# Performance work log

Measured on AMD Instinct MI355X. Metric: run time of the kernel, lower is better.

The kernel has to match this reference:

```python
import jax, jax.numpy as jnp
import numpy as np
from jax import lax

R = 1
EPS = 1e-4
K = 2 * R + 1


def _dir_kernels(r):
    k = 2 * r + 1
    ones = np.ones((k, k), np.float32)
    L = ones.copy(); L[:, r + 1:] = 0
    Rk = ones.copy(); Rk[:, :r] = 0
    U = ones.copy(); U[r + 1:, :] = 0
    D = ones.copy(); D[:r, :] = 0
    # NW/NE/SW/SE clone U/D BEFORE normalization (as in the torch code)
    NW = U.copy(); NW[:, r + 1:] = 0
    NE = U.copy(); NE[:, :r] = 0
    SW = D.copy(); SW[:, r + 1:] = 0
    SE = D.copy(); SE[:, :r] = 0
    half = (r + 1) * k          # normalizer for half windows
    quad = (r + 1) ** 2         # normalizer for quadrant windows
    L, Rk, U, D = L / half, Rk / half, U / half, D / half
    NW, NE, SW, SE = NW / quad, NE / quad, SW / quad, SE / quad
    return jnp.asarray(np.stack([L, Rk, U, D, NW, NE, SW, SE])[:, None])  # [8,1,k,k]


_DN = ('NCHW', 'OIHW', 'NCHW')


def _boxfilter(x, r):
    # replication pad + depthwise ones/(k*k) box filter; x: [N,3,H,W]
    k = 2 * r + 1
    xp = jnp.pad(x, ((0, 0), (0, 0), (r, r), (r, r)), mode='edge')
    w = jnp.full((3, 1, k, k), 1.0 / (k * k), dtype=x.dtype)
    return lax.conv_general_dilated(xp, w, (1, 1), 'VALID',
                                    dimension_numbers=_DN, feature_group_count=3)


def setup_inputs() -> dict:
    key = jax.random.key(0)
    k1, k2, k3 = jax.random.split(key, 3)
    lr_x = jax.random.uniform(k1, (1, 3, 2048, 2048), jnp.float32) * 255.0
    lr_y = jax.random.uniform(k2, (1, 3, 2048, 2048), jnp.float32) * 255.0
    hr_x = jax.random.uniform(k3, (1, 3, 4096, 4096), jnp.float32) * 255.0
    return {"lr_x": lr_x, "lr_y": lr_y, "hr_x": hr_x}


def reference(lr_x, lr_y, hr_x):
    # guided-filter coefficients on the low-res pair
    mean_x = _boxfilter(lr_x, R)
    mean_y = _boxfilter(lr_y, R)
    cov_xy = _boxfilter(lr_x * lr_y, R) - mean_x * mean_y
    var_x = _boxfilter(lr_x * lr_x, R) - mean_x * mean_x
    A = cov_xy / (var_x + EPS)            # [1,3,H,W]
    b = mean_y - A * mean_x               # [1,3,H,W]

    # treat channels as batch: [3,1,H,W]; 8 directional kernels at once
    Wd = _dir_kernels(R)                  # [8,1,k,k]
    A_ = A[0][:, None]
    b_ = b[0][:, None]
    im = lr_x[0][:, None]                 # [3,1,H,W]
    pad = [(R, R), (R, R)]
    convA = lax.conv_general_dilated(A_, Wd, (1, 1), pad, dimension_numbers=_DN)
    convb = lax.conv_general_dilated(b_, Wd, (1, 1), pad, dimension_numbers=_DN)
    d = convA * im + convb - im           # [3,8,H,W] directional residuals

    idx = jnp.argmin(jnp.abs(d), axis=1, keepdims=True)   # [3,1,H,W]
    dm = jnp.take_along_axis(d, idx, axis=1)              # best residual
    res = (dm + im).transpose(1, 0, 2, 3)                 # [1,3,H,W]
    # .int() truncation then clamp to [0,255], back to float
    return jnp.clip(jnp.trunc(res), 0.0, 255.0)
```

## Files before the change

### kernel.cpp

```cpp
#include <hip/hip_runtime.h>
#include <math.h>


#define TX 64
#define TY 16
#define SW (TX + 4)
#define SH (TY + 4)
#define AW (TX + 2)
#define AH (TY + 2)
#define NT 256

#define NA (AH * AW)
#define NV (AH * SW)
#define NS (SH * SW)
#define ITER_A ((NA + NT - 1) / NT)

__device__ __forceinline__ double fast_rcp(double v) {
#if __has_builtin(__builtin_amdgcn_rcp)
    double r = __builtin_amdgcn_rcp(v);
#else
    double r = 1.0 / v;
#endif
    double e = fma(-v, r, 1.0);
    r = fma(r, e, r);
    e = fma(-v, r, 1.0);
    r = fma(r, e, r);
    return r;
}

__global__ __launch_bounds__(NT) void fgf_fused_kernel(
    const float* __restrict__ x, const float* __restrict__ y,
    float* __restrict__ out, int H, int W)
{
    __shared__ float  sxs[SH][SW];
    __shared__ float  sys[SH][SW];
    __shared__ double sV[4][AH][SW];

    const int c   = blockIdx.z;
    const int ox0 = blockIdx.x * TX;
    const int oy0 = blockIdx.y * TY;
    const size_t plane = (size_t)H * (size_t)W;
    const float* xc = x + (size_t)c * plane;
    const float* yc = y + (size_t)c * plane;

    const int tid = threadIdx.y * 64 + threadIdx.x;

    for (int i = tid; i < NS; i += NT) {
        int ly = i / SW, lx = i - ly * SW;
        int gy = oy0 - 2 + ly;
        int gx = ox0 - 2 + lx;
        gy = gy < 0 ? 0 : (gy >= H ? H - 1 : gy);
        gx = gx < 0 ? 0 : (gx >= W ? W - 1 : gx);
        size_t gidx = (size_t)gy * W + gx;
        sxs[ly][lx] = xc[gidx];
        sys[ly][lx] = yc[gidx];
    }
    __syncthreads();

    for (int i = tid; i < NV; i += NT) {
        int ly = i / SW, lx = i - ly * SW;
        double x0 = (double)sxs[ly + 0][lx];
        double x1 = (double)sxs[ly + 1][lx];
        double x2 = (double)sxs[ly + 2][lx];
        double y0 = (double)sys[ly + 0][lx];
        double y1 = (double)sys[ly + 1][lx];
        double y2 = (double)sys[ly + 2][lx];
        sV[0][ly][lx] = (x0 + x1) + x2;
        sV[1][ly][lx] = (y0 + y1) + y2;
        sV[2][ly][lx] = fma(x2, y2, fma(x1, y1, x0 * y0));
        sV[3][ly][lx] = fma(x2, x2, fma(x1, x1, x0 * x0));
    }
    __syncthreads();

    const double EPS81 = 81.0 * 1.0e-4;
    const double INV9  = 1.0 / 9.0;
    double Abuf[ITER_A], Bbuf[ITER_A];
#pragma unroll
    for (int it = 0; it < ITER_A; it++) {
        int i = tid + it * NT;
        double Av = 0.0, Bv = 0.0;
        if (i < NA) {
            int ly = i / AW, lx = i - ly * AW;
            int ay = oy0 - 1 + ly;
            int ax = ox0 - 1 + lx;
            if (ay >= 0 && ay < H && ax >= 0 && ax < W) {
                double Sx  = (sV[0][ly][lx] + sV[0][ly][lx + 1]) + sV[0][ly][lx + 2];
                double Sy  = (sV[1][ly][lx] + sV[1][ly][lx + 1]) + sV[1][ly][lx + 2];
                double Sxy = (sV[2][ly][lx] + sV[2][ly][lx + 1]) + sV[2][ly][lx + 2];
                double Sxx = (sV[3][ly][lx] + sV[3][ly][lx + 1]) + sV[3][ly][lx + 2];
                double num = fma(9.0, Sxy, -(Sx * Sy));
                double den = fma(-Sx, Sx, fma(9.0, Sxx, EPS81));
                Av = num * fast_rcp(den);
                Bv = fma(-Av, Sx, Sy) * INV9;
            }
        }
        Abuf[it] = Av;
        Bbuf[it] = Bv;
    }
    __syncthreads();
#pragma unroll
    for (int it = 0; it < ITER_A; it++) {
        int i = tid + it * NT;
        if (i < NA) {
            int ly = i / AW, lx = i - ly * AW;
            sV[0][ly][lx] = Abuf[it];
            sV[1][ly][lx] = Bbuf[it];
        }
    }
    __syncthreads();

    double (*sA)[SW] = sV[0];
    double (*sB)[SW] = sV[1];

    const double I6 = 1.0 / 6.0;
    const int tx = threadIdx.x;
    const int g  = threadIdx.y;
    const int r0 = g * 4;
    const int xg = ox0 + tx;
    const bool xok = (xg < W);

    double tLA, tRA, tFA, mLA, mRA, mFA, pLA, pRA, pFA;
    double tLB, tRB, tFB, mLB, mRB, mFB, pLB, pRB, pFB;
    {
        double a0 = sA[r0 + 0][tx], a1 = sA[r0 + 0][tx + 1], a2 = sA[r0 + 0][tx + 2];
        double L0 = a0 + a1, R0 = a1 + a2, F0 = L0 + a2;
        a0 = sA[r0 + 1][tx]; a1 = sA[r0 + 1][tx + 1]; a2 = sA[r0 + 1][tx + 2];
        double L1 = a0 + a1, R1 = a1 + a2, F1 = L1 + a2;
        a0 = sA[r0 + 2][tx]; a1 = sA[r0 + 2][tx + 1]; a2 = sA[r0 + 2][tx + 2];
        double L2 = a0 + a1, R2 = a1 + a2, F2 = L2 + a2;
        tLA = L0 + L1; tRA = R0 + R1; tFA = F0 + F1;
        mLA = L1 + L2; mRA = R1 + R2; mFA = F1 + F2;
        pLA = L2; pRA = R2; pFA = F2;

        double b0 = sB[r0 + 0][tx], b1 = sB[r0 + 0][tx + 1], b2 = sB[r0 + 0][tx + 2];
        double M0 = b0 + b1, S0 = b1 + b2, G0 = M0 + b2;
        b0 = sB[r0 + 1][tx]; b1 = sB[r0 + 1][tx + 1]; b2 = sB[r0 + 1][tx + 2];
        double M1 = b0 + b1, S1 = b1 + b2, G1 = M1 + b2;
        b0 = sB[r0 + 2][tx]; b1 = sB[r0 + 2][tx + 1]; b2 = sB[r0 + 2][tx + 2];
        double M2 = b0 + b1, S2 = b1 + b2, G2 = M2 + b2;
        tLB = M0 + M1; tRB = S0 + S1; tFB = G0 + G1;
        mLB = M1 + M2; mRB = S1 + S2; mFB = G1 + G2;
        pLB = M2; pRB = S2; pFB = G2;
    }

#pragma unroll
    for (int step = 0; step < 4; step++) {
        const int r  = r0 + step;
        const int yg = oy0 + r;
        if (xok && yg < H) {
            double im  = (double)sxs[r + 2][tx + 2];
            double mim = -im;

            double sa[8] = { tLA + pLA, tRA + pRA, tFA, mFA, tLA, tRA, mLA, mRA };
            double sb[8] = { tLB + pLB, tRB + pRB, tFB, mFB, tLB, tRB, mLB, mRB };

            double best = 0.0;
#pragma unroll
            for (int k = 0; k < 8; k++) {
                double w = (k < 4) ? I6 : 0.25;
                double d = fma(w, fma(sa[k], im, sb[k]), mim);
                if (k == 0) best = d;
                else        best = (fabs(d) < fabs(best)) ? d : best;
            }

            double res = trunc(best + im);
            res = fmin(fmax(res, 0.0), 255.0);
            out[(size_t)c * plane + (size_t)yg * W + xg] = (float)res;
        }

        if (step < 3) {
            double n0 = sA[r + 3][tx], n1 = sA[r + 3][tx + 1], n2 = sA[r + 3][tx + 2];
            double nL = n0 + n1, nR = n1 + n2, nF = nL + n2;
            tLA = mLA; tRA = mRA; tFA = mFA;
            mLA = pLA + nL; mRA = pRA + nR; mFA = pFA + nF;
            pLA = nL; pRA = nR; pFA = nF;

            n0 = sB[r + 3][tx]; n1 = sB[r + 3][tx + 1]; n2 = sB[r + 3][tx + 2];
            nL = n0 + n1; nR = n1 + n2; nF = nL + n2;
            tLB = mLB; tRB = mRB; tFB = mFB;
            mLB = pLB + nL; mRB = pRB + nR; mFB = pFB + nF;
            pLB = nL; pRB = nR; pFB = nF;
        }
    }
}

extern "C" void kernel_launch(void* const* d_in, const int* in_sizes, int n_in,
                              void* d_out, int out_size, void* d_ws, size_t ws_size,
                              hipStream_t stream) {
    const float* lr_x = (const float*)d_in[0];
    const float* lr_y = (const float*)d_in[1];
    float* out = (float*)d_out;

    const int plane = in_sizes[0] / 3;
    const int H = (int)(0.5 + sqrt((double)plane));
    const int W = plane / H;

    dim3 block(64, 4, 1);
    dim3 grid((W + TX - 1) / TX, (H + TY - 1) / TY, 3);
    fgf_fused_kernel<<<grid, block, 0, stream>>>(lr_x, lr_y, out, H, W);
}
```

Measured before the change: 386.9 us.

## Halve tile height, drop float staging tiles, read vertical sums from global

```diff
diff --git a/kernel.cpp b/kernel.cpp
--- a/kernel.cpp
+++ b/kernel.cpp
@@ -3,16 +3,16 @@
 
 
 #define TX 64
-#define TY 16
+#define TY 8
 #define SW (TX + 4)
-#define SH (TY + 4)
+#define AH (TY + 2)
 #define AW (TX + 2)
-#define AH (TY + 2)
 #define NT 256
-
+#define STEPS 2
+
+#define NV (AH * SW)
 #define NA (AH * AW)
-#define NV (AH * SW)
-#define NS (SH * SW)
+#define ITER_V ((NV + NT - 1) / NT)
 #define ITER_A ((NA + NT - 1) / NT)
 
 __device__ __forceinline__ double fast_rcp(double v) {
@@ -28,12 +28,14 @@
     return r;
 }
 
-__global__ __launch_bounds__(NT) void fgf_fused_kernel(
+__device__ __forceinline__ int iclamp(int v, int lo, int hi) {
+    return v < lo ? lo : (v > hi ? hi : v);
+}
+
+__global__ __launch_bounds__(NT, 7) void fgf_fused_kernel(
     const float* __restrict__ x, const float* __restrict__ y,
     float* __restrict__ out, int H, int W)
 {
-    __shared__ float  sxs[SH][SW];
-    __shared__ float  sys[SH][SW];
     __shared__ double sV[4][AH][SW];
 
     const int c   = blockIdx.z;
@@ -43,32 +45,40 @@
     const float* xc = x + (size_t)c * plane;
     const float* yc = y + (size_t)c * plane;
 
-    const int tid = threadIdx.y * 64 + threadIdx.x;
-
-    for (int i = tid; i < NS; i += NT) {
-        int ly = i / SW, lx = i - ly * SW;
-        int gy = oy0 - 2 + ly;
-        int gx = ox0 - 2 + lx;
-        gy = gy < 0 ? 0 : (gy >= H ? H - 1 : gy);
-        gx = gx < 0 ? 0 : (gx >= W ? W - 1 : gx);
-        size_t gidx = (size_t)gy * W + gx;
-        sxs[ly][lx] = xc[gidx];
-        sys[ly][lx] = yc[gidx];
-    }
-    __syncthreads();
-
-    for (int i = tid; i < NV; i += NT) {
-        int ly = i / SW, lx = i - ly * SW;
-        double x0 = (double)sxs[ly + 0][lx];
-        double x1 = (double)sxs[ly + 1][lx];
-        double x2 = (double)sxs[ly + 2][lx];
-        double y0 = (double)sys[ly + 0][lx];
-        double y1 = (double)sys[ly + 1][lx];
-        double y2 = (double)sys[ly + 2][lx];
-        sV[0][ly][lx] = (x0 + x1) + x2;
-        sV[1][ly][lx] = (y0 + y1) + y2;
-        sV[2][ly][lx] = fma(x2, y2, fma(x1, y1, x0 * y0));
-        sV[3][ly][lx] = fma(x2, x2, fma(x1, x1, x0 * x0));
+    const int tx  = threadIdx.x;
+    const int g   = threadIdx.y;
+    const int tid = g * 64 + tx;
+    const int r0  = g * STEPS;
+    const int xg  = ox0 + tx;
+
+    float imf[STEPS];
+#pragma unroll
+    for (int s = 0; s < STEPS; s++) {
+        int yg = iclamp(oy0 + r0 + s, 0, H - 1);
+        int xp = iclamp(xg, 0, W - 1);
+        imf[s] = xc[(size_t)yg * W + xp];
+    }
+
+#pragma unroll
+    for (int it = 0; it < ITER_V; it++) {
+        int i = tid + it * NT;
+        if (i < NV) {
+            int ly = i / SW, lx = i - ly * SW;
+            int gx = iclamp(ox0 - 2 + lx, 0, W - 1);
+            int gy = oy0 - 2 + ly;
+            int g0 = iclamp(gy,     0, H - 1);
+            int g1 = iclamp(gy + 1, 0, H - 1);
+            int g2 = iclamp(gy + 2, 0, H - 1);
+            size_t i0 = (size_t)g0 * W + gx;
+            size_t i1 = (size_t)g1 * W + gx;
+            size_t i2 = (size_t)g2 * W + gx;
+            double x0 = (double)xc[i0], x1 = (double)xc[i1], x2 = (double)xc[i2];
+            double y0 = (double)yc[i0], y1 = (double)yc[i1], y2 = (double)yc[i2];
+            sV[0][ly][lx] = (x0 + x1) + x2;
+            sV[1][ly][lx] = (y0 + y1) + y2;
+            sV[2][ly][lx] = fma(x2, y2, fma(x1, y1, x0 * y0));
+            sV[3][ly][lx] = fma(x2, x2, fma(x1, x1, x0 * x0));
+        }
     }
     __syncthreads();
 
@@ -113,10 +123,6 @@
     double (*sB)[SW] = sV[1];
 
     const double I6 = 1.0 / 6.0;
-    const int tx = threadIdx.x;
-    const int g  = threadIdx.y;
-    const int r0 = g * 4;
-    const int xg = ox0 + tx;
     const bool xok = (xg < W);
 
     double tLA, tRA, tFA, mLA, mRA, mFA, pLA, pRA, pFA;
@@ -144,11 +150,11 @@
     }
 
 #pragma unroll
-    for (int step = 0; step < 4; step++) {
+    for (int step = 0; step < STEPS; step++) {
         const int r  = r0 + step;
         const int yg = oy0 + r;
         if (xok && yg < H) {
-            double im  = (double)sxs[r + 2][tx + 2];
+            double im  = (double)imf[step];
             double mim = -im;
 
             double sa[8] = { tLA + pLA, tRA + pRA, tFA, mFA, tLA, tRA, mLA, mRA };
@@ -168,7 +174,7 @@
             out[(size_t)c * plane + (size_t)yg * W + xg] = (float)res;
         }
 
-        if (step < 3) {
+        if (step < STEPS - 1) {
             double n0 = sA[r + 3][tx], n1 = sA[r + 3][tx + 1], n2 = sA[r + 3][tx + 2];
             double nL = n0 + n1, nR = n1 + n2, nF = nL + n2;
             tLA = mLA; tRA = mRA; tFA = mFA;
```

Measured after the change: 345.6 us. 1.12x faster.
